# Kernel optimization log

Hardware: AMD Instinct MI355X
Metric: run time of the kernel (lower is better)

## Reference

```python
import jax, jax.numpy as jnp
import numpy as np

B, N, D, Z, H = 256, 128, 256, 64, 128

def setup_inputs() -> dict:
    key = jax.random.key(0)
    ks = jax.random.split(key, 12)
    s = 0.02
    inp = {
        "h_obs": jax.random.normal(ks[0], (B, N, D), jnp.float32),
        "z": jax.random.normal(ks[1], (B, N, Z), jnp.float32),
        "start_pos": jax.random.normal(ks[2], (B, N, 2), jnp.float32),
        # input_proj: Linear(D+Z+2 -> H)
        "W_in": jax.random.normal(ks[3], (D + Z + 2, H), jnp.float32) * s,
        "b_in": jax.random.normal(ks[4], (H,), jnp.float32) * s,
        # GRUCell weights, PyTorch layout: [3H, H] rows ordered (r, z, n)
        "W_ih": jax.random.normal(ks[5], (3 * H, H), jnp.float32) * s,
        "b_ih": jax.random.normal(ks[6], (3 * H,), jnp.float32) * s,
        "W_hh": jax.random.normal(ks[7], (3 * H, H), jnp.float32) * s,
        "b_hh": jax.random.normal(ks[8], (3 * H,), jnp.float32) * s,
        # out_proj: Linear(H -> 2)
        "W_out": jax.random.normal(ks[9], (2, H), jnp.float32) * s,
        "b_out": jax.random.normal(ks[10], (2,), jnp.float32) * s,
        "pred_len": 30,
    }
    return inp

def _gru_cell(x, h, W_ih, b_ih, W_hh, b_hh):
    gi = x @ W_ih.T + b_ih            # [BN, 3H]
    gh = h @ W_hh.T + b_hh            # [BN, 3H]
    i_r, i_z, i_n = jnp.split(gi, 3, axis=-1)
    h_r, h_z, h_n = jnp.split(gh, 3, axis=-1)
    r = jax.nn.sigmoid(i_r + h_r)
    zg = jax.nn.sigmoid(i_z + h_z)
    n = jnp.tanh(i_n + r * h_n)
    return (1.0 - zg) * n + zg * h

def reference(h_obs, z, start_pos, W_in, b_in, W_ih, b_ih, W_hh, b_hh, W_out, b_out, pred_len):
    BN = B * N
    # h_obs and z are constant across steps: precompute their projection once.
    base = jnp.concatenate([h_obs, z], axis=-1).reshape(BN, D + Z)
    base_proj = base @ W_in[: D + Z] + b_in            # [BN, H]
    W_pos = W_in[D + Z:]                               # [2, H]

    state0 = jnp.zeros((BN, H), h_obs.dtype)
    pos0 = start_pos.reshape(BN, 2)

    def step(carry, _):
        state, pos = carry
        x = base_proj + pos @ W_pos                    # == input_proj(cat(h,z,pos))
        state = _gru_cell(x, state, W_ih, b_ih, W_hh, b_hh)
        delta = state @ W_out.T + b_out                # [BN, 2]
        pos = pos + delta
        return (state, pos), pos

    (_, _), traj = jax.lax.scan(step, (state0, pos0), None, length=pred_len)
    # traj: [T, BN, 2] -> [B, T, N, 2]
    return traj.reshape(pred_len, B, N, 2).transpose(1, 0, 2, 3)
```

## Files before the change

### kernel.cpp

```cpp
#include <hip/hip_runtime.h>
#include <hip/hip_bf16.h>


#define T_LEN 30
#define H_    128
#define G3_   384
#define KIN_  320
#define S2B   336
#define HB    (64*S2B)
#define TRAJ_OFF (2*HB)
#define LDS_BYTES (TRAJ_OFF + T_LEN*64*8)

#define SCL_RZ -1.44269504088896341f
#define SCL_N   2.88539008177792681f

typedef float  f32x4 __attribute__((ext_vector_type(4)));
typedef __bf16 b16x8 __attribute__((ext_vector_type(8)));
typedef unsigned u32x4 __attribute__((ext_vector_type(4)));

#define MFMA16(a,b,c) __builtin_amdgcn_mfma_f32_16x16x32_bf16((a),(b),(c),0,0,0)

__device__ __forceinline__ b16x8 pack8s(const float* p, float s){
  b16x8 r;
  #pragma unroll
  for (int i=0;i<8;i++) r[i] = (__bf16)(s*p[i]);
  return r;
}
__device__ __forceinline__ unsigned pk2(float a, float b){
  __bf16 x=(__bf16)a, y=(__bf16)b;
  unsigned short ux=__builtin_bit_cast(unsigned short,x);
  unsigned short uy=__builtin_bit_cast(unsigned short,y);
  return (unsigned)ux | ((unsigned)uy<<16);
}
__device__ __forceinline__ f32x4 unpk2(unsigned lo, unsigned hi){
  f32x4 r;
  r[0]=__builtin_bit_cast(float, lo<<16);
  r[1]=__builtin_bit_cast(float, lo&0xFFFF0000u);
  r[2]=__builtin_bit_cast(float, hi<<16);
  r[3]=__builtin_bit_cast(float, hi&0xFFFF0000u);
  return r;
}
__device__ __forceinline__ b16x8 fragu(unsigned v){
  u32x4 t = {v,0u,0u,0u};
  return __builtin_bit_cast(b16x8, t);
}

__global__ void prep_wc(const float* __restrict__ W_in, const float* __restrict__ W_ih,
                        __bf16* __restrict__ WcT){
  __shared__ float win[H_][16];
  int k0 = blockIdx.x << 4;
  for (int i=threadIdx.x; i<16*H_; i+=384){
    int kk = i>>7, m = i&127;
    win[m][kk] = W_in[(size_t)(k0+kk)*H_ + m];
  }
  __syncthreads();
  int j = threadIdx.x;
  const float* wr = W_ih + (size_t)j*H_;
  float acc[16];
  #pragma unroll
  for (int kk=0;kk<16;kk++) acc[kk]=0.f;
  for (int m=0;m<H_;m++){
    float wv = wr[m];
    #pragma unroll
    for (int kk=0;kk<16;kk++) acc[kk] = fmaf(wv, win[m][kk], acc[kk]);
  }
  float scl = (j < 2*H_) ? SCL_RZ : SCL_N;
  #pragma unroll
  for (int kk=0;kk<16;kk++) WcT[(size_t)j*KIN_ + k0 + kk] = (__bf16)(scl*acc[kk]);
}

__global__ void prep_vec(const float* __restrict__ W_in, const float* __restrict__ b_in,
                         const float* __restrict__ W_ih, const float* __restrict__ b_ih,
                         const float* __restrict__ b_hh, const float* __restrict__ b_out,
                         float* __restrict__ cvec, float* __restrict__ P2G){
  int j = threadIdx.x;
  const float* wr = W_ih + (size_t)j*H_;
  float s  = b_ih[j] + (j < 2*H_ ? b_hh[j] : 0.f);
  float p0 = 0.f, p1 = 0.f;
  #pragma unroll 8
  for (int m=0;m<H_;m++){
    float wv = wr[m];
    s  += b_in[m]*wv;
    p0 += W_in[(size_t)KIN_*H_ + m]*wv;
    p1 += W_in[(size_t)(KIN_+1)*H_ + m]*wv;
  }
  float scl = (j < 2*H_) ? SCL_RZ : SCL_N;
  float p0s = scl*p0, p1s = scl*p1;
  P2G[j] = p0s; P2G[G3_ + j] = p1s;
  cvec[j] = scl*s + b_out[0]*p0s + b_out[1]*p1s;
}

__global__ void prep_wt(const float* __restrict__ W_hh, const float* __restrict__ W_out,
                        const float* __restrict__ P2G, __bf16* __restrict__ WT){
  int jp = blockIdx.x;
  int set = jp >> 7, col = jp & 127;
  int j = (set==0) ? col : (set==1) ? H_+col : 2*H_+col;
  float p0 = P2G[j], p1 = P2G[G3_+j];
  int k = threadIdx.x;
  if (k >= 136) return;
  float v = 0.f;
  if (k < 128){
    if (set<=1)      v = SCL_RZ*W_hh[(size_t)j*H_+k] + p0*W_out[k] + p1*W_out[H_+k];
    else if (set==2) v = SCL_N *W_hh[(size_t)j*H_+k];
    else             v = p0*W_out[k] + p1*W_out[H_+k];
  } else if (k==128){ v = (set==2)? 0.f : p0; }
  else if (k==129){ v = (set==2)? 0.f : p1; }
  WT[(size_t)jp*136 + k] = (__bf16)v;
}

__global__ __launch_bounds__(512, 2)
void decoder(const float* __restrict__ h_obs, const float* __restrict__ zin,
             const float* __restrict__ start_pos,
             const float* __restrict__ b_hh, const float* __restrict__ W_out,
             const float* __restrict__ b_out,
             const __bf16* __restrict__ WcT, const float* __restrict__ cvec,
             const __bf16* __restrict__ WT, float* __restrict__ out)
{
  __shared__ __align__(16) char lds[LDS_BYTES];
  __bf16* stg = (__bf16*)lds;

  const int tid  = threadIdx.x;
  const int lane = tid & 63;
  const int w    = tid >> 6;
  const int l15  = lane & 15;
  const int lhi  = lane >> 4;
  const int R0   = blockIdx.x << 6;
  const int hcol = (w<<4) + l15;
  const int jr = hcol, jz = H_ + hcol, jn = 2*H_ + hcol;
  const int oc = l15 & 1;
  const bool desig = (w < 4);
  const int gd = w >> 1, md = w & 1;

  {
    const float4* src = reinterpret_cast<const float4*>(h_obs) + (size_t)R0*64;
    #pragma unroll
    for (int i=0;i<8;i++){
      int k = tid + (i<<9);
      float4 v = src[k];
      int r = k>>6, c = (k&63)<<2;
      __bf16* d = &stg[r*328 + c];
      d[0]=(__bf16)v.x; d[1]=(__bf16)v.y; d[2]=(__bf16)v.z; d[3]=(__bf16)v.w;
    }
    const float4* srcz = reinterpret_cast<const float4*>(zin) + (size_t)R0*16;
    #pragma unroll
    for (int i=0;i<2;i++){
      int k = tid + (i<<9);
      float4 v = srcz[k];
      int r = k>>4, c = 256 + ((k&15)<<2);
      __bf16* d = &stg[r*328 + c];
      d[0]=(__bf16)v.x; d[1]=(__bf16)v.y; d[2]=(__bf16)v.z; d[3]=(__bf16)v.w;
    }
  }

  const float bo0 = b_out[0], bo1 = b_out[1];
  const float bo  = oc ? bo1 : bo0;
  const float bhn = SCL_N * b_hh[2*H_ + hcol];
  const f32x4 bhnvec = (f32x4){bhn,bhn,bhn,bhn};

  b16x8 Br[4],Bz[4],Ban[4],Binn[4],Bo[4];
  #pragma unroll
  for (int kk=0;kk<4;kk++){
    const int ko = kk*32 + lhi*8;
    Br[kk]   = *reinterpret_cast<const b16x8*>(WT + (size_t)(      hcol)*136 + ko);
    Bz[kk]   = *reinterpret_cast<const b16x8*>(WT + (size_t)(128 + hcol)*136 + ko);
    Ban[kk]  = *reinterpret_cast<const b16x8*>(WT + (size_t)(256 + hcol)*136 + ko);
    Binn[kk] = *reinterpret_cast<const b16x8*>(WT + (size_t)(384 + hcol)*136 + ko);
    Bo[kk]   = pack8s(W_out + (size_t)oc*H_ + ko, 1.0f);
  }
  const b16x8 Br4 = fragu(lhi==0 ? *reinterpret_cast<const unsigned*>(WT + (size_t)(      hcol)*136 + 128) : 0u);
  const b16x8 Bz4 = fragu(lhi==0 ? *reinterpret_cast<const unsigned*>(WT + (size_t)(128 + hcol)*136 + 128) : 0u);
  const b16x8 Bi4 = fragu(lhi==0 ? *reinterpret_cast<const unsigned*>(WT + (size_t)(384 + hcol)*136 + 128) : 0u);

  float px[4]={0,0,0,0}, py[4]={0,0,0,0};
  if (desig){
    #pragma unroll
    for (int q=0;q<4;q++){
      int r = R0 + gd*32 + md*16 + lhi*4 + q;
      px[q] = start_pos[2*r]   - bo0;
      py[q] = start_pos[2*r+1] - bo1;
    }
  }

  __syncthreads();

  unsigned Gp[2][3][2][2];
  {
    f32x4 G[2][3][2];
    float cr = cvec[jr], cz = cvec[jz], cn = cvec[jn];
    #pragma unroll
    for (int g=0; g<2; g++){
      G[g][0][0] = (f32x4){cr,cr,cr,cr}; G[g][0][1] = G[g][0][0];
      G[g][1][0] = (f32x4){cz,cz,cz,cz}; G[g][1][1] = G[g][1][0];
      G[g][2][0] = (f32x4){cn,cn,cn,cn}; G[g][2][1] = G[g][2][0];
    }
    #pragma unroll 1
    for (int kk=0; kk<10; kk++){
      const int ko = (kk<<5) + (lhi<<3);
      b16x8 br = *reinterpret_cast<const b16x8*>(WcT + (size_t)jr*KIN_ + ko);
      b16x8 bz = *reinterpret_cast<const b16x8*>(WcT + (size_t)jz*KIN_ + ko);
      b16x8 bn = *reinterpret_cast<const b16x8*>(WcT + (size_t)jn*KIN_ + ko);
      #pragma unroll
      for (int g=0; g<2; g++){
        b16x8 a0 = *reinterpret_cast<const b16x8*>(&stg[(g*32   +l15)*328 + ko]);
        b16x8 a1 = *reinterpret_cast<const b16x8*>(&stg[(g*32+16+l15)*328 + ko]);
        G[g][0][0] = MFMA16(a0, br, G[g][0][0]); G[g][0][1] = MFMA16(a1, br, G[g][0][1]);
        G[g][1][0] = MFMA16(a0, bz, G[g][1][0]); G[g][1][1] = MFMA16(a1, bz, G[g][1][1]);
        G[g][2][0] = MFMA16(a0, bn, G[g][2][0]); G[g][2][1] = MFMA16(a1, bn, G[g][2][1]);
      }
    }
    #pragma unroll
    for (int g=0; g<2; g++)
      #pragma unroll
      for (int gate=0; gate<3; gate++)
        #pragma unroll
        for (int m=0; m<2; m++){
          Gp[g][gate][m][0] = pk2(G[g][gate][m][0], G[g][gate][m][1]);
          Gp[g][gate][m][1] = pk2(G[g][gate][m][2], G[g][gate][m][3]);
        }
  }
  __syncthreads();

  for (int i=tid; i<4096; i+=512){
    int r = i>>6, wq = i&63;
    *reinterpret_cast<unsigned*>(lds + r*S2B + wq*4) = 0u;
  }
  if (desig && l15==0){
    #pragma unroll
    for (int q=0;q<4;q++){
      int row = gd*32 + md*16 + lhi*4 + q;
      *reinterpret_cast<unsigned*>(lds + row*S2B + 256) = pk2(px[q], py[q]);
    }
  }

  float st[2][2][4];
  #pragma unroll
  for (int g=0;g<2;g++)
    #pragma unroll
    for (int m=0;m<2;m++)
      #pragma unroll
      for (int q=0;q<4;q++) st[g][m][q] = 0.f;

  const unsigned rdb = (unsigned)(l15*S2B + lhi*16);
  const f32x4 zero4 = (f32x4){0,0,0,0};

  int cur = 0;
  #pragma unroll 1
  for (int t=0; t<T_LEN; ++t){
    __syncthreads();
    const char* rb = lds + cur*HB;
    char*       wb = lds + (cur^1)*HB;

    #pragma unroll
    for (int g=0; g<2; ++g){
      const char* rg_ = rb + g*(32*S2B);
      char*       wg_ = wb + g*(32*S2B);

      f32x4 ar0 = unpk2(Gp[g][0][0][0], Gp[g][0][0][1]);
      f32x4 ar1 = unpk2(Gp[g][0][1][0], Gp[g][0][1][1]);
      f32x4 az0 = unpk2(Gp[g][1][0][0], Gp[g][1][0][1]);
      f32x4 az1 = unpk2(Gp[g][1][1][0], Gp[g][1][1][1]);
      f32x4 ai0 = unpk2(Gp[g][2][0][0], Gp[g][2][0][1]);
      f32x4 ai1 = unpk2(Gp[g][2][1][0], Gp[g][2][1][1]);
      f32x4 an0 = bhnvec, an1 = bhnvec;

      #pragma unroll
      for (int kk=0;kk<4;kk++){
        b16x8 a0 = *reinterpret_cast<const b16x8*>(rg_ + rdb + kk*64);
        b16x8 a1 = *reinterpret_cast<const b16x8*>(rg_ + rdb + 16*S2B + kk*64);
        ar0 = MFMA16(a0,Br[kk],ar0);   ar1 = MFMA16(a1,Br[kk],ar1);
        az0 = MFMA16(a0,Bz[kk],az0);   az1 = MFMA16(a1,Bz[kk],az1);
        an0 = MFMA16(a0,Ban[kk],an0);  an1 = MFMA16(a1,Ban[kk],an1);
        ai0 = MFMA16(a0,Binn[kk],ai0); ai1 = MFMA16(a1,Binn[kk],ai1);
      }
      {
        unsigned pp0 = *reinterpret_cast<const unsigned*>(rg_ + l15*S2B + 256);
        unsigned pp1 = *reinterpret_cast<const unsigned*>(rg_ + (16+l15)*S2B + 256);
        b16x8 a40 = fragu(lhi==0 ? pp0 : 0u);
        b16x8 a41 = fragu(lhi==0 ? pp1 : 0u);
        ar0 = MFMA16(a40,Br4,ar0); ar1 = MFMA16(a41,Br4,ar1);
        az0 = MFMA16(a40,Bz4,az0); az1 = MFMA16(a41,Bz4,az1);
        ai0 = MFMA16(a40,Bi4,ai0); ai1 = MFMA16(a41,Bi4,ai1);
      }

      if (desig && gd == g){
        f32x4 d;
        if (md==0){
          b16x8 f0 = *reinterpret_cast<const b16x8*>(rg_ + rdb);
          d = MFMA16(f0,Bo[0],zero4);
          #pragma unroll
          for (int kk=1;kk<4;kk++){
            b16x8 fk = *reinterpret_cast<const b16x8*>(rg_ + rdb + kk*64);
            d = MFMA16(fk,Bo[kk],d);
          }
        } else {
          b16x8 f0 = *reinterpret_cast<const b16x8*>(rg_ + rdb + 16*S2B);
          d = MFMA16(f0,Bo[0],zero4);
          #pragma unroll
          for (int kk=1;kk<4;kk++){
            b16x8 fk = *reinterpret_cast<const b16x8*>(rg_ + rdb + 16*S2B + kk*64);
            d = MFMA16(fk,Bo[kk],d);
          }
        }
        #pragma unroll
        for (int q=0;q<4;q++){
          float dme  = d[q] + bo;
          float doth = __shfl_xor(dme, 1);
          px[q] += oc ? doth : dme;
          py[q] += oc ? dme  : doth;
        }
        if (l15==0){
          #pragma unroll
          for (int q=0;q<4;q++){
            int row = md*16 + lhi*4 + q;
            if (t > 0){
              float2 v; v.x = px[q]; v.y = py[q];
              *reinterpret_cast<float2*>(lds + TRAJ_OFF + ((t-1)*64 + g*32 + row)*8) = v;
            }
            *reinterpret_cast<unsigned*>(wg_ + row*S2B + 256) = pk2(px[q], py[q]);
          }
        }
      }

      #pragma unroll
      for (int m=0;m<2;m++){
        f32x4 Ar = m? ar1:ar0, Az = m? az1:az0, An = m? an1:an0, Ai = m? ai1:ai0;
        #pragma unroll
        for (int q=0;q<4;q++){
          float rgt = __builtin_amdgcn_rcpf(1.f + __builtin_amdgcn_exp2f(Ar[q]));
          float zgt = __builtin_amdgcn_rcpf(1.f + __builtin_amdgcn_exp2f(Az[q]));
          float na  = fmaf(rgt, An[q], Ai[q]);
          float nn  = fmaf(-2.f, __builtin_amdgcn_rcpf(1.f + __builtin_amdgcn_exp2f(na)), 1.f);
          float h   = fmaf(zgt, st[g][m][q] - nn, nn);
          st[g][m][q] = h;
          *reinterpret_cast<__bf16*>(wg_ + (m*16+lhi*4+q)*S2B + hcol*2) = (__bf16)h;
        }
      }
    }
    cur ^= 1;
  }

  __syncthreads();
  if (desig){
    const char* rg_ = lds + cur*HB + gd*(32*S2B);
    f32x4 d;
    {
      b16x8 f0 = *reinterpret_cast<const b16x8*>(rg_ + (md*16+l15)*S2B + lhi*16);
      d = MFMA16(f0,Bo[0],zero4);
      #pragma unroll
      for (int kk=1;kk<4;kk++){
        b16x8 fk = *reinterpret_cast<const b16x8*>(rg_ + (md*16+l15)*S2B + lhi*16 + kk*64);
        d = MFMA16(fk,Bo[kk],d);
      }
    }
    #pragma unroll
    for (int q=0;q<4;q++){
      float dme  = d[q] + bo;
      float doth = __shfl_xor(dme, 1);
      px[q] += oc ? doth : dme;
      py[q] += oc ? dme  : doth;
    }
    if (l15==0){
      #pragma unroll
      for (int q=0;q<4;q++){
        int row = gd*32 + md*16 + lhi*4 + q;
        float2 v; v.x = px[q]; v.y = py[q];
        *reinterpret_cast<float2*>(lds + TRAJ_OFF + ((T_LEN-1)*64 + row)*8) = v;
      }
    }
  }

  __syncthreads();
  {
    const float* traj = reinterpret_cast<const float*>(lds + TRAJ_OFF);
    const size_t ob  = ((size_t)(R0>>7)*T_LEN)<<8;
    const int    n02 = (R0 & 127)<<1;
    for (int i=tid; i<T_LEN*128; i+=512){
      int tt = i>>7, j = i&127;
      out[ob + (size_t)tt*256 + n02 + j] = traj[i];
    }
  }
}

extern "C" void kernel_launch(void* const* d_in, const int* in_sizes, int n_in,
                              void* d_out, int out_size, void* d_ws, size_t ws_size,
                              hipStream_t stream) {
  const float* h_obs     = (const float*)d_in[0];
  const float* z         = (const float*)d_in[1];
  const float* start_pos = (const float*)d_in[2];
  const float* W_in      = (const float*)d_in[3];
  const float* b_in      = (const float*)d_in[4];
  const float* W_ih      = (const float*)d_in[5];
  const float* b_ih      = (const float*)d_in[6];
  const float* W_hh      = (const float*)d_in[7];
  const float* b_hh      = (const float*)d_in[8];
  const float* W_out     = (const float*)d_in[9];
  const float* b_out     = (const float*)d_in[10];

  char* ws = (char*)d_ws;
  __bf16* WcT  = (__bf16*)ws;
  float*  cvec = (float*)(ws + 245760);
  float*  P2G  = (float*)(ws + 247296);
  __bf16* WT   = (__bf16*)(ws + 250368);

  prep_wc <<<20,  384, 0, stream>>>(W_in, W_ih, WcT);
  prep_vec<<<1,   384, 0, stream>>>(W_in, b_in, W_ih, b_ih, b_hh, b_out, cvec, P2G);
  prep_wt <<<512, 192, 0, stream>>>(W_hh, W_out, P2G, WT);
  decoder <<<512, 512, 0, stream>>>(h_obs, z, start_pos, b_hh, W_out, b_out,
                                    WcT, cvec, WT, (float*)d_out);
}
```

Before: 324.3 us.

## Process 128 rows per block and fuse output projection into GRU loop

Each block now handles 128 rows instead of 64 and the grid is halved to 256 blocks. All eight waves now take part in the position update. The output-projection MFMAs are folded into the recurrent k-loop, reusing the A fragments already loaded, with the bias carried in the accumulator. The LDS row stride shrinks to 272 bytes. This saves weight-fragment loads per row and removes the separate projection pass, but it doubles per-wave serial work per step. The larger LDS footprint likely limits residency to one block per CU, which reduces latency hiding.

```diff
diff --git a/kernel.cpp b/kernel.cpp
--- a/kernel.cpp
+++ b/kernel.cpp
@@ -6,10 +6,10 @@
 #define H_    128
 #define G3_   384
 #define KIN_  320
-#define S2B   336
-#define HB    (64*S2B)
+#define S2B   272
+#define HB    (128*S2B)
 #define TRAJ_OFF (2*HB)
-#define LDS_BYTES (TRAJ_OFF + T_LEN*64*8)
+#define LDS_BYTES (TRAJ_OFF + T_LEN*128*8)
 
 #define SCL_RZ -1.44269504088896341f
 #define SCL_N   2.88539008177792681f
@@ -124,17 +124,16 @@
   const int w    = tid >> 6;
   const int l15  = lane & 15;
   const int lhi  = lane >> 4;
-  const int R0   = blockIdx.x << 6;
+  const int R0   = blockIdx.x << 7;
   const int hcol = (w<<4) + l15;
   const int jr = hcol, jz = H_ + hcol, jn = 2*H_ + hcol;
   const int oc = l15 & 1;
-  const bool desig = (w < 4);
   const int gd = w >> 1, md = w & 1;
 
   {
     const float4* src = reinterpret_cast<const float4*>(h_obs) + (size_t)R0*64;
     #pragma unroll
-    for (int i=0;i<8;i++){
+    for (int i=0;i<16;i++){
       int k = tid + (i<<9);
       float4 v = src[k];
       int r = k>>6, c = (k&63)<<2;
@@ -143,7 +142,7 @@
     }
     const float4* srcz = reinterpret_cast<const float4*>(zin) + (size_t)R0*16;
     #pragma unroll
-    for (int i=0;i<2;i++){
+    for (int i=0;i<4;i++){
       int k = tid + (i<<9);
       float4 v = srcz[k];
       int r = k>>4, c = 256 + ((k&15)<<2);
@@ -156,6 +155,53 @@
   const float bo  = oc ? bo1 : bo0;
   const float bhn = SCL_N * b_hh[2*H_ + hcol];
   const f32x4 bhnvec = (f32x4){bhn,bhn,bhn,bhn};
+  const f32x4 bovec  = (f32x4){bo,bo,bo,bo};
+
+  float px[4], py[4];
+  #pragma unroll
+  for (int q=0;q<4;q++){
+    int r = R0 + (gd<<5) + (md<<4) + (lhi<<2) + q;
+    px[q] = start_pos[2*r]   - bo0;
+    py[q] = start_pos[2*r+1] - bo1;
+  }
+
+  __syncthreads();
+
+  unsigned Gp[4][3][2][2];
+  {
+    f32x4 G[4][3][2];
+    float cr = cvec[jr], cz = cvec[jz], cn = cvec[jn];
+    #pragma unroll
+    for (int g=0; g<4; g++){
+      G[g][0][0] = (f32x4){cr,cr,cr,cr}; G[g][0][1] = G[g][0][0];
+      G[g][1][0] = (f32x4){cz,cz,cz,cz}; G[g][1][1] = G[g][1][0];
+      G[g][2][0] = (f32x4){cn,cn,cn,cn}; G[g][2][1] = G[g][2][0];
+    }
+    #pragma unroll 1
+    for (int kk=0; kk<10; kk++){
+      const int ko = (kk<<5) + (lhi<<3);
+      b16x8 br = *reinterpret_cast<const b16x8*>(WcT + (size_t)jr*KIN_ + ko);
+      b16x8 bz = *reinterpret_cast<const b16x8*>(WcT + (size_t)jz*KIN_ + ko);
+      b16x8 bn = *reinterpret_cast<const b16x8*>(WcT + (size_t)jn*KIN_ + ko);
+      #pragma unroll
+      for (int g=0; g<4; g++){
+        b16x8 a0 = *reinterpret_cast<const b16x8*>(&stg[(g*32   +l15)*328 + ko]);
+        b16x8 a1 = *reinterpret_cast<const b16x8*>(&stg[(g*32+16+l15)*328 + ko]);
+        G[g][0][0] = MFMA16(a0, br, G[g][0][0]); G[g][0][1] = MFMA16(a1, br, G[g][0][1]);
+        G[g][1][0] = MFMA16(a0, bz, G[g][1][0]); G[g][1][1] = MFMA16(a1, bz, G[g][1][1]);
+        G[g][2][0] = MFMA16(a0, bn, G[g][2][0]); G[g][2][1] = MFMA16(a1, bn, G[g][2][1]);
+      }
+    }
+    #pragma unroll
+    for (int g=0; g<4; g++)
+      #pragma unroll
+      for (int gate=0; gate<3; gate++)
+        #pragma unroll
+        for (int m=0; m<2; m++){
+          Gp[g][gate][m][0] = pk2(G[g][gate][m][0], G[g][gate][m][1]);
+          Gp[g][gate][m][1] = pk2(G[g][gate][m][2], G[g][gate][m][3]);
+        }
+  }
 
   b16x8 Br[4],Bz[4],Ban[4],Binn[4],Bo[4];
   #pragma unroll
@@ -171,77 +217,29 @@
   const b16x8 Bz4 = fragu(lhi==0 ? *reinterpret_cast<const unsigned*>(WT + (size_t)(128 + hcol)*136 + 128) : 0u);
   const b16x8 Bi4 = fragu(lhi==0 ? *reinterpret_cast<const unsigned*>(WT + (size_t)(384 + hcol)*136 + 128) : 0u);
 
-  float px[4]={0,0,0,0}, py[4]={0,0,0,0};
-  if (desig){
+  __syncthreads();
+
+  for (int i=tid; i<8192; i+=512){
+    int r = i>>6, dw = i&63;
+    *reinterpret_cast<unsigned*>(lds + r*S2B + dw*4) = 0u;
+  }
+  if (l15==0){
     #pragma unroll
     for (int q=0;q<4;q++){
-      int r = R0 + gd*32 + md*16 + lhi*4 + q;
-      px[q] = start_pos[2*r]   - bo0;
-      py[q] = start_pos[2*r+1] - bo1;
-    }
-  }
-
-  __syncthreads();
-
-  unsigned Gp[2][3][2][2];
-  {
-    f32x4 G[2][3][2];
-    float cr = cvec[jr], cz = cvec[jz], cn = cvec[jn];
-    #pragma unroll
-    for (int g=0; g<2; g++){
-      G[g][0][0] = (f32x4){cr,cr,cr,cr}; G[g][0][1] = G[g][0][0];
-      G[g][1][0] = (f32x4){cz,cz,cz,cz}; G[g][1][1] = G[g][1][0];
-      G[g][2][0] = (f32x4){cn,cn,cn,cn}; G[g][2][1] = G[g][2][0];
-    }
-    #pragma unroll 1
-    for (int kk=0; kk<10; kk++){
-      const int ko = (kk<<5) + (lhi<<3);
-      b16x8 br = *reinterpret_cast<const b16x8*>(WcT + (size_t)jr*KIN_ + ko);
-      b16x8 bz = *reinterpret_cast<const b16x8*>(WcT + (size_t)jz*KIN_ + ko);
-      b16x8 bn = *reinterpret_cast<const b16x8*>(WcT + (size_t)jn*KIN_ + ko);
-      #pragma unroll
-      for (int g=0; g<2; g++){
-        b16x8 a0 = *reinterpret_cast<const b16x8*>(&stg[(g*32   +l15)*328 + ko]);
-        b16x8 a1 = *reinterpret_cast<const b16x8*>(&stg[(g*32+16+l15)*328 + ko]);
-        G[g][0][0] = MFMA16(a0, br, G[g][0][0]); G[g][0][1] = MFMA16(a1, br, G[g][0][1]);
-        G[g][1][0] = MFMA16(a0, bz, G[g][1][0]); G[g][1][1] = MFMA16(a1, bz, G[g][1][1]);
-        G[g][2][0] = MFMA16(a0, bn, G[g][2][0]); G[g][2][1] = MFMA16(a1, bn, G[g][2][1]);
-      }
-    }
-    #pragma unroll
-    for (int g=0; g<2; g++)
-      #pragma unroll
-      for (int gate=0; gate<3; gate++)
-        #pragma unroll
-        for (int m=0; m<2; m++){
-          Gp[g][gate][m][0] = pk2(G[g][gate][m][0], G[g][gate][m][1]);
-          Gp[g][gate][m][1] = pk2(G[g][gate][m][2], G[g][gate][m][3]);
-        }
-  }
-  __syncthreads();
-
-  for (int i=tid; i<4096; i+=512){
-    int r = i>>6, wq = i&63;
-    *reinterpret_cast<unsigned*>(lds + r*S2B + wq*4) = 0u;
-  }
-  if (desig && l15==0){
-    #pragma unroll
-    for (int q=0;q<4;q++){
-      int row = gd*32 + md*16 + lhi*4 + q;
+      int row = (gd<<5) + (md<<4) + (lhi<<2) + q;
       *reinterpret_cast<unsigned*>(lds + row*S2B + 256) = pk2(px[q], py[q]);
     }
   }
 
-  float st[2][2][4];
-  #pragma unroll
-  for (int g=0;g<2;g++)
+  float st[4][2][4];
+  #pragma unroll
+  for (int g=0;g<4;g++)
     #pragma unroll
     for (int m=0;m<2;m++)
       #pragma unroll
       for (int q=0;q<4;q++) st[g][m][q] = 0.f;
 
   const unsigned rdb = (unsigned)(l15*S2B + lhi*16);
-  const f32x4 zero4 = (f32x4){0,0,0,0};
 
   int cur = 0;
   #pragma unroll 1
@@ -251,9 +249,10 @@
     char*       wb = lds + (cur^1)*HB;
 
     #pragma unroll
-    for (int g=0; g<2; ++g){
+    for (int g=0; g<4; ++g){
       const char* rg_ = rb + g*(32*S2B);
       char*       wg_ = wb + g*(32*S2B);
+      const bool own = (gd == g);
 
       f32x4 ar0 = unpk2(Gp[g][0][0][0], Gp[g][0][0][1]);
       f32x4 ar1 = unpk2(Gp[g][0][1][0], Gp[g][0][1][1]);
@@ -262,6 +261,7 @@
       f32x4 ai0 = unpk2(Gp[g][2][0][0], Gp[g][2][0][1]);
       f32x4 ai1 = unpk2(Gp[g][2][1][0], Gp[g][2][1][1]);
       f32x4 an0 = bhnvec, an1 = bhnvec;
+      f32x4 dAcc = bovec;
 
       #pragma unroll
       for (int kk=0;kk<4;kk++){
@@ -271,6 +271,10 @@
         az0 = MFMA16(a0,Bz[kk],az0);   az1 = MFMA16(a1,Bz[kk],az1);
         an0 = MFMA16(a0,Ban[kk],an0);  an1 = MFMA16(a1,Ban[kk],an1);
         ai0 = MFMA16(a0,Binn[kk],ai0); ai1 = MFMA16(a1,Binn[kk],ai1);
+        if (own){
+          b16x8 am = md ? a1 : a0;
+          dAcc = MFMA16(am, Bo[kk], dAcc);
+        }
       }
       {
         unsigned pp0 = *reinterpret_cast<const unsigned*>(rg_ + l15*S2B + 256);
@@ -282,28 +286,10 @@
         ai0 = MFMA16(a40,Bi4,ai0); ai1 = MFMA16(a41,Bi4,ai1);
       }
 
-      if (desig && gd == g){
-        f32x4 d;
-        if (md==0){
-          b16x8 f0 = *reinterpret_cast<const b16x8*>(rg_ + rdb);
-          d = MFMA16(f0,Bo[0],zero4);
-          #pragma unroll
-          for (int kk=1;kk<4;kk++){
-            b16x8 fk = *reinterpret_cast<const b16x8*>(rg_ + rdb + kk*64);
-            d = MFMA16(fk,Bo[kk],d);
-          }
-        } else {
-          b16x8 f0 = *reinterpret_cast<const b16x8*>(rg_ + rdb + 16*S2B);
-          d = MFMA16(f0,Bo[0],zero4);
-          #pragma unroll
-          for (int kk=1;kk<4;kk++){
-            b16x8 fk = *reinterpret_cast<const b16x8*>(rg_ + rdb + 16*S2B + kk*64);
-            d = MFMA16(fk,Bo[kk],d);
-          }
-        }
+      if (own){
         #pragma unroll
         for (int q=0;q<4;q++){
-          float dme  = d[q] + bo;
+          float dme  = dAcc[q];
           float doth = __shfl_xor(dme, 1);
           px[q] += oc ? doth : dme;
           py[q] += oc ? dme  : doth;
@@ -311,12 +297,12 @@
         if (l15==0){
           #pragma unroll
           for (int q=0;q<4;q++){
-            int row = md*16 + lhi*4 + q;
+            int row = (gd<<5) + (md<<4) + (lhi<<2) + q;
             if (t > 0){
               float2 v; v.x = px[q]; v.y = py[q];
-              *reinterpret_cast<float2*>(lds + TRAJ_OFF + ((t-1)*64 + g*32 + row)*8) = v;
+              *reinterpret_cast<float2*>(lds + TRAJ_OFF + ((t-1)*128 + row)*8) = v;
             }
-            *reinterpret_cast<unsigned*>(wg_ + row*S2B + 256) = pk2(px[q], py[q]);
+            *reinterpret_cast<unsigned*>(wb + row*S2B + 256) = pk2(px[q], py[q]);
           }
         }
       }
@@ -332,7 +318,7 @@
           float nn  = fmaf(-2.f, __builtin_amdgcn_rcpf(1.f + __builtin_amdgcn_exp2f(na)), 1.f);
           float h   = fmaf(zgt, st[g][m][q] - nn, nn);
           st[g][m][q] = h;
-          *reinterpret_cast<__bf16*>(wg_ + (m*16+lhi*4+q)*S2B + hcol*2) = (__bf16)h;
+          *reinterpret_cast<__bf16*>(wg_ + ((m<<4)+(lhi<<2)+q)*S2B + hcol*2) = (__bf16)h;
         }
       }
     }
@@ -340,21 +326,18 @@
   }
 
   __syncthreads();
-  if (desig){
+  {
     const char* rg_ = lds + cur*HB + gd*(32*S2B);
-    f32x4 d;
-    {
-      b16x8 f0 = *reinterpret_cast<const b16x8*>(rg_ + (md*16+l15)*S2B + lhi*16);
-      d = MFMA16(f0,Bo[0],zero4);
-      #pragma unroll
-      for (int kk=1;kk<4;kk++){
-        b16x8 fk = *reinterpret_cast<const b16x8*>(rg_ + (md*16+l15)*S2B + lhi*16 + kk*64);
-        d = MFMA16(fk,Bo[kk],d);
-      }
+    const unsigned dbase = (unsigned)((md*16 + l15)*S2B + lhi*16);
+    f32x4 d = bovec;
+    #pragma unroll
+    for (int kk=0;kk<4;kk++){
+      b16x8 fk = *reinterpret_cast<const b16x8*>(rg_ + dbase + kk*64);
+      d = MFMA16(fk, Bo[kk], d);
     }
     #pragma unroll
     for (int q=0;q<4;q++){
-      float dme  = d[q] + bo;
+      float dme  = d[q];
       float doth = __shfl_xor(dme, 1);
       px[q] += oc ? doth : dme;
       py[q] += oc ? dme  : doth;
@@ -362,22 +345,18 @@
     if (l15==0){
       #pragma unroll
       for (int q=0;q<4;q++){
-        int row = gd*32 + md*16 + lhi*4 + q;
+        int row = (gd<<5) + (md<<4) + (lhi<<2) + q;
         float2 v; v.x = px[q]; v.y = py[q];
-        *reinterpret_cast<float2*>(lds + TRAJ_OFF + ((T_LEN-1)*64 + row)*8) = v;
+        *reinterpret_cast<float2*>(lds + TRAJ_OFF + ((T_LEN-1)*128 + row)*8) = v;
       }
     }
   }
 
   __syncthreads();
   {
-    const float* traj = reinterpret_cast<const float*>(lds + TRAJ_OFF);
-    const size_t ob  = ((size_t)(R0>>7)*T_LEN)<<8;
-    const int    n02 = (R0 & 127)<<1;
-    for (int i=tid; i<T_LEN*128; i+=512){
-      int tt = i>>7, j = i&127;
-      out[ob + (size_t)tt*256 + n02 + j] = traj[i];
-    }
+    const float* trajf = reinterpret_cast<const float*>(lds + TRAJ_OFF);
+    const size_t ob = (size_t)blockIdx.x * (T_LEN*256);
+    for (int i=tid; i<T_LEN*256; i+=512) out[ob + i] = trajf[i];
   }
 }
 
@@ -405,6 +384,6 @@
   prep_wc <<<20,  384, 0, stream>>>(W_in, W_ih, WcT);
   prep_vec<<<1,   384, 0, stream>>>(W_in, b_in, W_ih, b_ih, b_hh, b_out, cvec, P2G);
   prep_wt <<<512, 192, 0, stream>>>(W_hh, W_out, P2G, WT);
-  decoder <<<512, 512, 0, stream>>>(h_obs, z, start_pos, b_hh, W_out, b_out,
+  decoder <<<256, 512, 0, stream>>>(h_obs, z, start_pos, b_hh, W_out, b_out,
                                     WcT, cvec, WT, (float*)d_out);
 }
```

Measured after the change: 357.3 us. 1.1x slower.
